# Optimization experiments

Measured on AMD Instinct MI355X. Metric: run time of the kernel, lower is better.

## Reference

```python
import jax, jax.numpy as jnp
import numpy as np

B, S, H, I = 4, 2048, 2048, 5504


def setup_inputs() -> dict:
    key = jax.random.key(0)
    k1, k2, k3, k4 = jax.random.split(key, 4)
    scale = 0.02
    return {
        "hidden_state": jax.random.normal(k1, (B, S, H), dtype=jnp.float32),
        "w_gate": jax.random.normal(k2, (I, H), dtype=jnp.float32) * scale,  # gate_proj.weight [out,in]
        "w_up": jax.random.normal(k3, (I, H), dtype=jnp.float32) * scale,    # up_proj.weight
        "w_down": jax.random.normal(k4, (H, I), dtype=jnp.float32) * scale,  # down_proj.weight
    }


def reference(hidden_state, w_gate, w_up, w_down):
    # SwiGLU: act(x W_g^T) * (x W_u^T)
    gate = jax.nn.silu(jnp.einsum("bsh,ih->bsi", hidden_state, w_gate))
    up = jnp.einsum("bsh,ih->bsi", hidden_state, w_up)
    intermediate = gate * up  # [B,S,I]

    # Neuron impacts. Original broadcasts (B,I,1)*(1,I,H) and sums over H;
    # algebraically identical to s[b,i] * ||w_up[i,:]||^2, which we use to
    # avoid materializing the [B,I,H] tensor. Same math, same result.
    s = jnp.sum(intermediate ** 2, axis=1)          # sum over seq dim -> [B,I]
    row_sq = jnp.sum(w_up ** 2, axis=-1)            # [I]
    impacts = jnp.sqrt(s * row_sq[None, :])          # [B,I]

    out = jnp.einsum("bsi,hi->bsh", intermediate, w_down)  # down_proj
    return out, impacts
```

## Files before the change

kernel.cpp:

```cpp
#include <hip/hip_runtime.h>
#include <stdint.h>
#include <stddef.h>

typedef __attribute__((ext_vector_type(8))) short short8;
typedef __attribute__((ext_vector_type(4))) float f32x4;
typedef unsigned short u16;

#define B_ 4
#define S_ 2048
#define H_ 2048
#define I_ 5504
#define M_ 8192

__device__ __forceinline__ u16 f2bf(float f) {
  uint32_t u = __float_as_uint(f);
  u += 0x7fff + ((u >> 16) & 1);
  return (u16)(u >> 16);
}

#define GLOAD_LDS16(src, dst)                                                            \
  __builtin_amdgcn_global_load_lds((const __attribute__((address_space(1))) void*)(src), \
                                   (__attribute__((address_space(3))) void*)(dst), 16, 0, 0)

__global__ __launch_bounds__(256) void cvt_f32_bf16(const float* __restrict__ in,
                                                    u16* __restrict__ out, int n4) {
  int i = blockIdx.x * 256 + threadIdx.x;
  if (i < n4) {
    float4 v = ((const float4*)in)[i];
    ushort4 o;
    o.x = f2bf(v.x); o.y = f2bf(v.y); o.z = f2bf(v.z); o.w = f2bf(v.w);
    ((ushort4*)out)[i] = o;
  }
}

__global__ __launch_bounds__(256) void cvt_wcat(const float* __restrict__ wg,
                                                const float* __restrict__ wu,
                                                u16* __restrict__ wcat) {
  const int i = blockIdx.x * 256 + threadIdx.x;
  const int f = i * 4;
  const int r = f >> 11;
  const int c = f & 2047;
  const int srcrow = (r >> 5) * 16 + (r & 15);
  const float* src = (((r >> 4) & 1) ? wu : wg) + (size_t)srcrow * 2048 + c;
  float4 v = *(const float4*)src;
  ushort4 o;
  o.x = f2bf(v.x); o.y = f2bf(v.y); o.z = f2bf(v.z); o.w = f2bf(v.w);
  *(ushort4*)(wcat + (size_t)r * 2048 + c) = o;
}

__device__ __forceinline__ void stage_half(const u16* __restrict__ mbase, int ld, int k0,
                                           char* slot, int tid) {
#pragma unroll
  for (int i = 0; i < 2; ++i) {
    const int f = tid * 16 + i * 8192;
    const int row = f >> 6;
    const int cl = (f >> 4) & 3;
    const int col = k0 + 8 * (cl ^ ((row >> 1) & 3));
    GLOAD_LDS16(mbase + (size_t)row * ld + col, slot + ((tid >> 6) * 1024 + i * 8192));
  }
}

#define PH_BAR asm volatile("s_barrier" ::: "memory")
#define WAIT_LGK0                                        \
  {                                                      \
    asm volatile("s_waitcnt lgkmcnt(0)" ::: "memory");   \
    __builtin_amdgcn_sched_barrier(0);                   \
  }

#define MM2(av, bx, by, N0, N1)                                                                 \
  {                                                                                             \
    __builtin_amdgcn_s_setprio(1);                                                              \
    _Pragma("unroll") for (int m = 0; m < 8; ++m) {                                             \
      acc[m][N0] = __builtin_amdgcn_mfma_f32_16x16x32_bf16(av[m], bx, acc[m][N0], 0, 0, 0);     \
      acc[m][N1] = __builtin_amdgcn_mfma_f32_16x16x32_bf16(av[m], by, acc[m][N1], 0, 0, 0);     \
    }                                                                                           \
    __builtin_amdgcn_s_setprio(0);                                                              \
  }

template <int EPI>
__global__ __launch_bounds__(512, 1) void gemm8(const u16* __restrict__ A,
                                                const u16* __restrict__ Bm, const int K,
                                                const int NT, float* __restrict__ outf,
                                                u16* __restrict__ inter, float* __restrict__ s) {
  __shared__ __align__(16) char lds_raw[131072 + 512];

  const int nwg = gridDim.x;
  const int cpx = nwg >> 3;
  const int swz = (blockIdx.x & 7) * cpx + (blockIdx.x >> 3);
  const int mt = swz / NT;
  const int nt = swz % NT;

  const int tid = threadIdx.x;
  const int lane = tid & 63;
  const int wid = tid >> 6;
  const int wr = wid >> 2;
  const int wc = wid & 3;
  const int l15 = lane & 15;

  if (tid < 128) ((float*)(lds_raw + 131072))[tid] = 0.f;

  const int chunkx = (l15 >> 1) & 3;
  const int aoff = (wr * 128 + l15) * 64 + (((lane >> 4) ^ chunkx) << 4);
  const int boff = (wc * 64 + l15) * 64 + (((lane >> 4) ^ chunkx) << 4);

  const u16* Abase = A + (size_t)(mt * 256) * K;
  const u16* Bbase = Bm + (size_t)(nt * 256) * K;

#define STG(v, q)                                                   \
  stage_half((q) < 2 ? Abase : Bbase, K, (v) * 64 + ((q) & 1) * 32, \
             lds_raw + (((v) & 1) * 65536 + (q) * 16384), tid)
#define RDA8(dst, c, ks)                                         \
  _Pragma("unroll") for (int m = 0; m < 8; ++m) dst[m] =         \
      *(const short8*)(lds_raw + (c) * 65536 + (ks) * 16384 + aoff + m * 1024);
#define RDB(dst, c, ks, n) \
  dst = *(const short8*)(lds_raw + (c) * 65536 + 32768 + (ks) * 16384 + boff + (n) * 1024);

  f32x4 acc[8][4] = {};
  short8 a[8], a2[8];
  short8 bx, by;

  const int T = K >> 6;

  STG(0, 0); STG(0, 1); STG(0, 2); STG(0, 3);
  STG(1, 0); STG(1, 2); STG(1, 1);
  asm volatile("s_waitcnt vmcnt(6)" ::: "memory");
  PH_BAR;

#pragma unroll 1
  for (int t = 0; t < T; ++t) {
    const int c = t & 1;
    const bool s1 = (t + 1 < T);
    const bool s2 = (t + 2 < T);
    RDA8(a, c, 0);
    RDB(bx, c, 0, 0);
    RDB(by, c, 0, 1);
    if (s1) STG(t + 1, 3);
    PH_BAR;
    WAIT_LGK0;
    MM2(a, bx, by, 0, 1);
    PH_BAR;
    RDB(bx, c, 0, 2);
    RDB(by, c, 0, 3);
    if (s2) STG(t + 2, 0);
    PH_BAR;
    WAIT_LGK0;
    MM2(a, bx, by, 2, 3);
    PH_BAR;
    RDA8(a2, c, 1);
    RDB(bx, c, 1, 0);
    RDB(by, c, 1, 1);
    if (s2) STG(t + 2, 2);
    PH_BAR;
    WAIT_LGK0;
    MM2(a2, bx, by, 0, 1);
    PH_BAR;
    RDB(bx, c, 1, 2);
    RDB(by, c, 1, 3);
    if (s2) STG(t + 2, 1);
    PH_BAR;
    if (s2) {
      asm volatile("s_waitcnt vmcnt(6) lgkmcnt(0)" ::: "memory");
    } else {
      asm volatile("s_waitcnt vmcnt(0) lgkmcnt(0)" ::: "memory");
    }
    __builtin_amdgcn_sched_barrier(0);
    MM2(a2, bx, by, 2, 3);
    PH_BAR;
  }

  const int r0 = mt * 256 + wr * 128 + (lane >> 4) * 4;
  if constexpr (EPI == 0) {
    const int c0 = nt * 256 + wc * 64 + l15;
#pragma unroll
    for (int m = 0; m < 8; ++m)
#pragma unroll
      for (int n = 0; n < 4; ++n)
#pragma unroll
        for (int j = 0; j < 4; ++j)
          outf[(size_t)(r0 + m * 16 + j) * 2048 + (c0 + n * 16)] = acc[m][n][j];
  } else {
    float* s_tile = (float*)(lds_raw + 131072);
    const int c0 = nt * 128 + wc * 32 + l15;
    float sp0 = 0.f, sp1 = 0.f;
#pragma unroll
    for (int m = 0; m < 8; ++m) {
#pragma unroll
      for (int j = 0; j < 4; ++j) {
        {
          const float g = acc[m][0][j], u = acc[m][1][j];
          const float v = (g / (1.f + __expf(-g))) * u;
          sp0 += v * v;
          inter[(size_t)(r0 + m * 16 + j) * I_ + c0] = f2bf(v);
        }
        {
          const float g = acc[m][2][j], u = acc[m][3][j];
          const float v = (g / (1.f + __expf(-g))) * u;
          sp1 += v * v;
          inter[(size_t)(r0 + m * 16 + j) * I_ + (c0 + 16)] = f2bf(v);
        }
      }
    }
    atomicAdd(&s_tile[wc * 32 + l15], sp0);
    atomicAdd(&s_tile[wc * 32 + 16 + l15], sp1);
    __syncthreads();
    if (tid < 128) atomicAdd(&s[(mt >> 3) * I_ + nt * 128 + tid], s_tile[tid]);
  }
#undef STG
#undef RDA8
#undef RDB
}

__global__ __launch_bounds__(256) void rowsq_impacts(const float* __restrict__ wu,
                                                     const float* __restrict__ s,
                                                     float* __restrict__ imp) {
  const int i = blockIdx.x;
  const int tid = threadIdx.x;
  const float4* row = (const float4*)(wu + (size_t)i * H_);
  float acc = 0.f;
#pragma unroll
  for (int t = 0; t < 2; ++t) {
    float4 v = row[tid + t * 256];
    acc += v.x * v.x + v.y * v.y + v.z * v.z + v.w * v.w;
  }
#pragma unroll
  for (int off = 32; off > 0; off >>= 1) acc += __shfl_down(acc, off, 64);
  __shared__ float wsum[4];
  if ((tid & 63) == 0) wsum[tid >> 6] = acc;
  __syncthreads();
  if (tid == 0) {
    const float rs = wsum[0] + wsum[1] + wsum[2] + wsum[3];
#pragma unroll
    for (int b = 0; b < 4; ++b) imp[b * I_ + i] = sqrtf(s[b * I_ + i] * rs);
  }
}

extern "C" void kernel_launch(void* const* d_in, const int* in_sizes, int n_in,
                              void* d_out, int out_size, void* d_ws, size_t ws_size,
                              hipStream_t stream) {
  const float* x = (const float*)d_in[0];
  const float* wg = (const float*)d_in[1];
  const float* wu = (const float*)d_in[2];
  const float* wd = (const float*)d_in[3];
  float* out = (float*)d_out;
  float* imp = out + (size_t)M_ * H_;

  char* ws = (char*)d_ws;
  u16* xb = (u16*)(ws);
  u16* wcatb = (u16*)(ws + 33554432);
  u16* wdb = (u16*)(ws + 78643200);
  u16* interb = (u16*)(ws + 101187584);
  float* s = (float*)(ws + 191365120);

  cvt_f32_bf16<<<16384, 256, 0, stream>>>(x, xb, (M_ * H_) / 4);
  cvt_wcat<<<22016, 256, 0, stream>>>(wg, wu, wcatb);
  cvt_f32_bf16<<<11008, 256, 0, stream>>>(wd, wdb, (H_ * I_) / 4);
  hipMemsetAsync(s, 0, (size_t)B_ * I_ * sizeof(float), stream);

  gemm8<1><<<1376, 512, 0, stream>>>(xb, wcatb, 2048, 43, nullptr, interb, s);
  gemm8<0><<<256, 512, 0, stream>>>(interb, wdb, 5504, 8, out, nullptr, nullptr);
  rowsq_impacts<<<I_, 256, 0, stream>>>(wu, s, imp);
}
```

Baseline: 765.6 us.

## Halve barriers per k-step, drop sched_barriers, precompute staging offsets

Removes the barrier after each MFMA block and the sched_barrier fences in the GEMM main loop, leaving one barrier per phase placed after the LDS wait. B fragments now go to separate registers per phase, so the compiler can overlap reads with the MFMAs. Global/LDS staging offsets are computed once outside the loop instead of every call. Fewer barriers risk LDS hazards, since a buffer may be overwritten while slower waves still read it, and the extra registers raise pressure.

New measurement: 713.2 us. -6.8%, faster.

```diff
diff --git a/kernel.cpp b/kernel.cpp
--- a/kernel.cpp
+++ b/kernel.cpp
@@ -48,33 +48,17 @@
   *(ushort4*)(wcat + (size_t)r * 2048 + c) = o;
 }
 
-__device__ __forceinline__ void stage_half(const u16* __restrict__ mbase, int ld, int k0,
-                                           char* slot, int tid) {
-#pragma unroll
-  for (int i = 0; i < 2; ++i) {
-    const int f = tid * 16 + i * 8192;
-    const int row = f >> 6;
-    const int cl = (f >> 4) & 3;
-    const int col = k0 + 8 * (cl ^ ((row >> 1) & 3));
-    GLOAD_LDS16(mbase + (size_t)row * ld + col, slot + ((tid >> 6) * 1024 + i * 8192));
-  }
-}
-
+#define WAITLGK0 asm volatile("s_waitcnt lgkmcnt(0)" ::: "memory")
 #define PH_BAR asm volatile("s_barrier" ::: "memory")
-#define WAIT_LGK0                                        \
-  {                                                      \
-    asm volatile("s_waitcnt lgkmcnt(0)" ::: "memory");   \
-    __builtin_amdgcn_sched_barrier(0);                   \
-  }
-
-#define MM2(av, bx, by, N0, N1)                                                                 \
-  {                                                                                             \
-    __builtin_amdgcn_s_setprio(1);                                                              \
-    _Pragma("unroll") for (int m = 0; m < 8; ++m) {                                             \
-      acc[m][N0] = __builtin_amdgcn_mfma_f32_16x16x32_bf16(av[m], bx, acc[m][N0], 0, 0, 0);     \
-      acc[m][N1] = __builtin_amdgcn_mfma_f32_16x16x32_bf16(av[m], by, acc[m][N1], 0, 0, 0);     \
-    }                                                                                           \
-    __builtin_amdgcn_s_setprio(0);                                                              \
+
+#define MM2(av, bx, by, N0, N1)                                                             \
+  {                                                                                         \
+    __builtin_amdgcn_s_setprio(1);                                                          \
+    _Pragma("unroll") for (int m = 0; m < 8; ++m) {                                         \
+      acc[m][N0] = __builtin_amdgcn_mfma_f32_16x16x32_bf16(av[m], bx, acc[m][N0], 0, 0, 0); \
+      acc[m][N1] = __builtin_amdgcn_mfma_f32_16x16x32_bf16(av[m], by, acc[m][N1], 0, 0, 0); \
+    }                                                                                       \
+    __builtin_amdgcn_s_setprio(0);                                                          \
   }
 
 template <int EPI>
@@ -106,18 +90,31 @@
   const u16* Abase = A + (size_t)(mt * 256) * K;
   const u16* Bbase = Bm + (size_t)(nt * 256) * K;
 
-#define STG(v, q)                                                   \
-  stage_half((q) < 2 ? Abase : Bbase, K, (v) * 64 + ((q) & 1) * 32, \
-             lds_raw + (((v) & 1) * 65536 + (q) * 16384), tid)
-#define RDA8(dst, c, ks)                                         \
-  _Pragma("unroll") for (int m = 0; m < 8; ++m) dst[m] =         \
+  int goff[2], loff[2];
+#pragma unroll
+  for (int i = 0; i < 2; ++i) {
+    const int f = tid * 16 + i * 8192;
+    const int row = f >> 6;
+    const int cl = (f >> 4) & 3;
+    goff[i] = row * K + 8 * (cl ^ ((row >> 1) & 3));
+    loff[i] = (tid >> 6) * 1024 + i * 8192;
+  }
+
+#define STG(v, q)                                                              \
+  {                                                                            \
+    const u16* _b = ((q) < 2 ? Abase : Bbase) + (v) * 64 + ((q) & 1) * 32;     \
+    char* _s = lds_raw + (((v) & 1) * 65536 + (q) * 16384);                    \
+    GLOAD_LDS16(_b + goff[0], _s + loff[0]);                                   \
+    GLOAD_LDS16(_b + goff[1], _s + loff[1]);                                   \
+  }
+#define RDA8(dst, c, ks)                                 \
+  _Pragma("unroll") for (int m = 0; m < 8; ++m) dst[m] = \
       *(const short8*)(lds_raw + (c) * 65536 + (ks) * 16384 + aoff + m * 1024);
 #define RDB(dst, c, ks, n) \
   dst = *(const short8*)(lds_raw + (c) * 65536 + 32768 + (ks) * 16384 + boff + (n) * 1024);
 
   f32x4 acc[8][4] = {};
   short8 a[8], a2[8];
-  short8 bx, by;
 
   const int T = K >> 6;
 
@@ -131,41 +128,37 @@
     const int c = t & 1;
     const bool s1 = (t + 1 < T);
     const bool s2 = (t + 2 < T);
+    short8 b0x, b0y, b1x, b1y, b2x, b2y, b3x, b3y;
     RDA8(a, c, 0);
-    RDB(bx, c, 0, 0);
-    RDB(by, c, 0, 1);
+    RDB(b0x, c, 0, 0);
+    RDB(b0y, c, 0, 1);
     if (s1) STG(t + 1, 3);
-    PH_BAR;
-    WAIT_LGK0;
-    MM2(a, bx, by, 0, 1);
-    PH_BAR;
-    RDB(bx, c, 0, 2);
-    RDB(by, c, 0, 3);
+    WAITLGK0;
+    PH_BAR;
+    MM2(a, b0x, b0y, 0, 1);
+    RDB(b1x, c, 0, 2);
+    RDB(b1y, c, 0, 3);
     if (s2) STG(t + 2, 0);
-    PH_BAR;
-    WAIT_LGK0;
-    MM2(a, bx, by, 2, 3);
-    PH_BAR;
+    WAITLGK0;
+    PH_BAR;
+    MM2(a, b1x, b1y, 2, 3);
     RDA8(a2, c, 1);
-    RDB(bx, c, 1, 0);
-    RDB(by, c, 1, 1);
+    RDB(b2x, c, 1, 0);
+    RDB(b2y, c, 1, 1);
     if (s2) STG(t + 2, 2);
-    PH_BAR;
-    WAIT_LGK0;
-    MM2(a2, bx, by, 0, 1);
-    PH_BAR;
-    RDB(bx, c, 1, 2);
-    RDB(by, c, 1, 3);
+    WAITLGK0;
+    PH_BAR;
+    MM2(a2, b2x, b2y, 0, 1);
+    RDB(b3x, c, 1, 2);
+    RDB(b3y, c, 1, 3);
     if (s2) STG(t + 2, 1);
-    PH_BAR;
     if (s2) {
       asm volatile("s_waitcnt vmcnt(6) lgkmcnt(0)" ::: "memory");
     } else {
       asm volatile("s_waitcnt vmcnt(0) lgkmcnt(0)" ::: "memory");
     }
-    __builtin_amdgcn_sched_barrier(0);
-    MM2(a2, bx, by, 2, 3);
-    PH_BAR;
+    PH_BAR;
+    MM2(a2, b3x, b3y, 2, 3);
   }
 
   const int r0 = mt * 256 + wr * 128 + (lane >> 4) * 4;
```
